# Kernel tuning notes

Hardware: AMD Instinct MI355X
Metric: run time of the kernel (lower is better)

The kernel has to match this reference:

```python
import jax, jax.numpy as jnp
import numpy as np

B, S, IN, H, D, NH, L, C = 32, 512, 3, 64, 128, 8, 4, 5
NSUB = 10          # euler substeps per interval: dt = interval/10 for these inputs
MAX_CONSEC = 50    # max_consecutive_steps in torch code
DH = D // NH
EPS = 1e-5


def _ln(x, g, b):
    m = x.mean(-1, keepdims=True)
    v = ((x - m) ** 2).mean(-1, keepdims=True)
    return (x - m) / jnp.sqrt(v + EPS) * g + b


def setup_inputs():
    key = jax.random.key(0)
    ks = jax.random.split(key, 24)
    def g(i, shape, scale=0.05):
        return jax.random.normal(ks[i], shape, dtype=jnp.float32) * scale
    dts = jax.random.uniform(ks[0], (B, S), minval=0.001, maxval=0.05, dtype=jnp.float32)
    times = jnp.cumsum(dts, axis=1)  # strictly increasing, positive
    return dict(
        time_series=jax.random.normal(ks[1], (B, S, IN), dtype=jnp.float32),
        times=times,
        noise=jax.random.normal(ks[2], (S, NSUB, B, H), dtype=jnp.float32),
        mask=jnp.ones((B, S), dtype=bool),
        enc_w=g(3, (IN, H)), enc_b=jnp.zeros((H,)),
        enc_g=jnp.ones((H,)), enc_beta=jnp.zeros((H,)),
        dw1=g(4, (H + 1, 2 * H)), db1=jnp.zeros((2 * H,)),
        dw2=g(5, (2 * H, H)), db2=jnp.zeros((H,)),
        dw3=g(6, (H, H)), db3=jnp.zeros((H,)),
        aw1=g(7, (1, H)), ab1=jnp.zeros((H,)),
        aw2=g(8, (H, H)), ab2=jnp.zeros((H,)),
        bw1=g(9, (1, H)), bb1=jnp.zeros((H,)),
        bw2=g(10, (H, H)), bb2=jnp.zeros((H,)),
        min_diff=jnp.float32(0.1),
        in_w=g(11, (H, D)), in_b=jnp.zeros((D,)),
        wq=g(12, (L, D, D)), bq=jnp.zeros((L, D)),
        wk=g(13, (L, D, D)), bk=jnp.zeros((L, D)),
        wv=g(14, (L, D, D)), bv=jnp.zeros((L, D)),
        wo=g(15, (L, D, D)), bo=jnp.zeros((L, D)),
        ln1_g=jnp.ones((L, D)), ln1_b=jnp.zeros((L, D)),
        ln2_g=jnp.ones((L, D)), ln2_b=jnp.zeros((L, D)),
        fw1=g(16, (L, D, 4 * D)), fb1=jnp.zeros((L, 4 * D)),
        fw2=g(17, (L, 4 * D, D)), fb2=jnp.zeros((L, D)),
        cw1=g(18, (D, D // 2)), cb1=jnp.zeros((D // 2,)),
        cw2=g(19, (D // 2, C)), cb2=jnp.zeros((C,)),
    )


def reference(time_series, times, noise, mask, enc_w, enc_b, enc_g, enc_beta,
              dw1, db1, dw2, db2, dw3, db3, aw1, ab1, aw2, ab2, bw1, bb1, bw2, bb2,
              min_diff, in_w, in_b, wq, bq, wk, bk, wv, bv, wo, bo,
              ln1_g, ln1_b, ln2_g, ln2_b, fw1, fb1, fw2, fb2, cw1, cb1, cw2, cb2):
    # feature encoder: Linear -> LayerNorm -> ReLU (dropout off / eval)
    enc = jax.nn.relu(_ln(time_series @ enc_w + enc_b, enc_g, enc_beta))  # (B,S,H)

    def drift(t, y):
        tcol = jnp.full((y.shape[0], 1), t, dtype=y.dtype)
        ty = jnp.concatenate([y, tcol], axis=1)
        h1 = jnp.tanh(ty @ dw1 + db1)
        h2 = jnp.tanh(h1 @ dw2 + db2)
        return h2 @ dw3 + db3

    def diffusion(t, y):
        tcol = jnp.full((y.shape[0], 1), t, dtype=y.dtype)
        A = jax.nn.softplus(jnp.tanh(tcol @ aw1 + ab1) @ aw2 + ab2)
        Bt = jnp.tanh(jnp.tanh(tcol @ bw1 + bb1) @ bw2 + bb2)
        return A + Bt * y + jnp.abs(min_diff)

    t_seq = times[0]  # torch code uses batch element 0's timestamps for sdeint

    def step(carry, xs):
        state, consec = carry
        enc_i, t_prev, t_cur, dW = xs  # dW: (NSUB,B,H) standard normals
        h = (t_cur - t_prev) / NSUB    # dt = interval/10 (< self.dt for these inputs)
        sqh = jnp.sqrt(h)
        y0 = jax.lax.stop_gradient(state)  # torch detaches y0 at every step

        def sub(y, kw):
            k, dw = kw
            t = t_prev + k * h
            return y + drift(t, y) * h + diffusion(t, y) * sqh * dw, None

        y_int, _ = jax.lax.scan(sub, y0, (jnp.arange(NSUB, dtype=jnp.float32), dW))
        skip = consec >= MAX_CONSEC
        out = jnp.where(skip, enc_i, y_int)
        consec = jnp.where(skip, jnp.int32(0), consec + 1)
        return (out, consec), out

    y0 = enc[:, 0]
    xs = (jnp.swapaxes(enc, 0, 1)[1:], t_seq[:-1], t_seq[1:], noise[1:])
    _, traj = jax.lax.scan(step, (y0, jnp.int32(0)), xs)
    sde_features = jnp.concatenate([y0[:, None], jnp.swapaxes(traj, 0, 1)], axis=1)  # (B,S,H)

    mf = mask.astype(sde_features.dtype)
    sde_features = sde_features * mf[..., None]  # MaskedSequenceProcessor.apply_mask

    # ContiFormer (post-LN transformer encoder) over SDE features
    x = sde_features @ in_w + in_b  # (B,S,D)
    neg = jnp.asarray(-1e9, x.dtype)
    for l in range(L):
        q = (x @ wq[l] + bq[l]).reshape(B, S, NH, DH)
        k = (x @ wk[l] + bk[l]).reshape(B, S, NH, DH)
        v = (x @ wv[l] + bv[l]).reshape(B, S, NH, DH)
        scores = jnp.einsum('bqhd,bkhd->bhqk', q, k) / np.float32(np.sqrt(DH))
        scores = jnp.where(mask[:, None, None, :], scores, neg)
        att = jax.nn.softmax(scores, axis=-1)
        o = jnp.einsum('bhqk,bkhd->bqhd', att, v).reshape(B, S, D) @ wo[l] + bo[l]
        x = _ln(x + o, ln1_g[l], ln1_b[l])
        f = jax.nn.relu(x @ fw1[l] + fb1[l]) @ fw2[l] + fb2[l]
        x = _ln(x + f, ln2_g[l], ln2_b[l])
    pooled = (x * mf[..., None]).sum(1) / jnp.maximum(mf.sum(1, keepdims=True), 1.0)

    logits = jax.nn.relu(pooled @ cw1 + cb1) @ cw2 + cb2
    return logits, sde_features
```

## Files before the change

kernel.cpp:

```cpp
#include <hip/hip_runtime.h>
#include <hip/hip_bf16.h>


typedef __attribute__((ext_vector_type(8))) short short8;
typedef __attribute__((ext_vector_type(4))) float f32x4;

static constexpr int OFF_TS      = 0;
static constexpr int OFF_TIMES   = 49152;
static constexpr int OFF_ENCW    = 65536;
static constexpr int OFF_ENCB    = 65728;
static constexpr int OFF_ENCG    = 65792;
static constexpr int OFF_ENCBETA = 65856;
static constexpr int OFF_DW1     = 65920;
static constexpr int OFF_DB1     = 74240;
static constexpr int OFF_DW2     = 74368;
static constexpr int OFF_DB2     = 82560;
static constexpr int OFF_DW3     = 82624;
static constexpr int OFF_DB3     = 86720;
static constexpr int OFF_AW1     = 86784;
static constexpr int OFF_AB1     = 86848;
static constexpr int OFF_AW2     = 86912;
static constexpr int OFF_AB2     = 91008;
static constexpr int OFF_BW1     = 91072;
static constexpr int OFF_BB1     = 91136;
static constexpr int OFF_BW2     = 91200;
static constexpr int OFF_BB2     = 95296;
static constexpr int OFF_MD      = 95360;
static constexpr int OFF_INW     = 95424;
static constexpr int OFF_INB     = 103616;
static constexpr int OFF_WQ      = 103744;
static constexpr int OFF_BQ      = 169280;
static constexpr int OFF_WK      = 169792;
static constexpr int OFF_BK      = 235328;
static constexpr int OFF_WV      = 235840;
static constexpr int OFF_BV      = 301376;
static constexpr int OFF_WO      = 301888;
static constexpr int OFF_BO      = 367424;
static constexpr int OFF_LN1G    = 367936;
static constexpr int OFF_LN1B    = 368448;
static constexpr int OFF_LN2G    = 368960;
static constexpr int OFF_LN2B    = 369472;
static constexpr int OFF_FW1     = 369984;
static constexpr int OFF_FB1     = 632128;
static constexpr int OFF_FW2     = 634176;
static constexpr int OFF_FB2     = 896320;
static constexpr int OFF_CW1     = 896832;
static constexpr int OFF_CB1     = 905024;
static constexpr int OFF_CW2     = 905088;
static constexpr int OFF_CB2     = 905472;
static constexpr int OFF_FLAG    = 905536;
static constexpr int OFF_ENC     = 905600;
static constexpr int OFF_COEFA   = 3002752;
static constexpr int OFF_COEFB   = 3329792;
static constexpr int OFF_B1C     = 3656832;
static constexpr int OFF_X       = 4310912;
static constexpr int OFF_XBF     = 6408064;
static constexpr int OFF_QKVBF   = 7456640;
static constexpr int OFF_OBF     = 10602368;
static constexpr int OFF_HBF     = 11650944;
static constexpr int OFF_SDEBF   = 15845248;
static constexpr int OFF_WQKVT   = 16369536;
static constexpr int OFF_WOT     = 16467840;
static constexpr int OFF_FW1T    = 16500608;
static constexpr int OFF_FW2T    = 16631680;
static constexpr int OFF_INWT    = 16762752;
static constexpr int OFF_BQKV    = 16766848;
static constexpr int OFF_TMP     = 23185280;

struct PtrPack { const void* p[45]; };

__device__ inline float wsum64(float v) {
#pragma unroll
  for (int off = 32; off > 0; off >>= 1) v += __shfl_xor(v, off, 64);
  return v;
}

__device__ inline float fast_tanh(float x) {
  x = fminf(fmaxf(x, -15.f), 15.f);
  float e = __expf(2.f * x);
  return (e - 1.f) / (e + 1.f);
}

__device__ inline float tanh5(float x) {
  float e = __builtin_amdgcn_exp2f(x * 2.88539008f);
  return 1.f - 2.f * __builtin_amdgcn_rcpf(e + 1.f);
}

__device__ inline float bfdec(unsigned short h) {
  return __uint_as_float(((unsigned)h) << 16);
}

__device__ inline short f2bf(float f) {
  unsigned u = __float_as_uint(f);
  return (short)((u + 0x7FFFu + ((u >> 16) & 1u)) >> 16);
}

__device__ inline void lds_barrier() {
  asm volatile("s_waitcnt lgkmcnt(0)\ns_barrier" ::: "memory");
}

__global__ __launch_bounds__(256) void ingest_kernel(PtrPack pk, float* __restrict__ W) {
  const int NE = 43;
  const int cnt[NE] = {49152,16384,192,64,64,64,8320,128,8192,64,4096,64,64,64,4096,64,
                       64,64,4096,64,1,8192,128,65536,512,65536,512,65536,512,65536,512,
                       512,512,512,512,262144,2048,262144,512,8192,64,320,5};
  const int src[NE] = {0,1,4,5,6,7,8,9,10,11,12,13,14,15,16,17,18,19,20,21,22,23,24,
                       25,26,27,28,29,30,31,32,33,34,35,36,37,38,39,40,41,42,43,44};
  const int dst[NE] = {OFF_TS,OFF_TIMES,OFF_ENCW,OFF_ENCB,OFF_ENCG,OFF_ENCBETA,OFF_DW1,
                       OFF_DB1,OFF_DW2,OFF_DB2,OFF_DW3,OFF_DB3,OFF_AW1,OFF_AB1,OFF_AW2,
                       OFF_AB2,OFF_BW1,OFF_BB1,OFF_BW2,OFF_BB2,OFF_MD,OFF_INW,OFF_INB,
                       OFF_WQ,OFF_BQ,OFF_WK,OFF_BK,OFF_WV,OFF_BV,OFF_WO,OFF_BO,
                       OFF_LN1G,OFF_LN1B,OFF_LN2G,OFF_LN2B,OFF_FW1,OFF_FB1,OFF_FW2,
                       OFF_FB2,OFF_CW1,OFF_CB1,OFF_CW2,OFF_CB2};
  const unsigned* eg = (const unsigned*)pk.p[6];
  int gmode = (eg[0] == 0x3F803F80u) ? 1 : 0;

  __shared__ int isbf[NE];
  if (threadIdx.x < NE) {
    int k = threadIdx.x;
    int f = gmode;
    if (gmode) {
      const unsigned short* us = (const unsigned short*)pk.p[src[k]];
      int n = cnt[k] < 32 ? cnt[k] : 32;
      for (int i = 0; i < n; ++i) {
        unsigned short h = us[i];
        if (h & 0x7FFF) {
          float a = fabsf(bfdec(h));
          if (!(a > 1e-20f && a < 1e4f)) { f = 0; break; }
        }
      }
    }
    isbf[k] = f;
  }
  __syncthreads();

  int gid = blockIdx.x * 256 + threadIdx.x;
  int stride = gridDim.x * 256;
  if (gid == 0) {
    int nf = gmode;
    if (gmode) {
      const unsigned short* us = (const unsigned short*)pk.p[2];
      for (int i = 0; i < 32; ++i) {
        unsigned short h = us[i];
        if (h & 0x7FFF) {
          float a = fabsf(bfdec(h));
          if (!(a > 1e-20f && a < 1e4f)) { nf = 0; break; }
        }
      }
    }
    ((int*)W)[OFF_FLAG] = nf;
  }
  for (int k = 0; k < NE; ++k) {
    int n = cnt[k];
    float* dp = W + dst[k];
    if (isbf[k]) {
      const unsigned short* us = (const unsigned short*)pk.p[src[k]];
      for (int e = gid; e < n; e += stride) dp[e] = bfdec(us[e]);
    } else {
      const float* fs = (const float*)pk.p[src[k]];
      for (int e = gid; e < n; e += stride) dp[e] = fs[e];
    }
  }
}

__global__ __launch_bounds__(256) void prep_kernel(float* __restrict__ W) {
  short* wqkvT = (short*)(W + OFF_WQKVT);
  short* woT   = (short*)(W + OFF_WOT);
  short* fw1T  = (short*)(W + OFF_FW1T);
  short* fw2T  = (short*)(W + OFF_FW2T);
  short* inwT  = (short*)(W + OFF_INWT);
  float* bqkv  = W + OFF_BQKV;
  int gid = blockIdx.x * 256 + threadIdx.x;
  int stride = gridDim.x * 256;
  for (int e = gid; e < 4096; e += stride) W[OFF_TMP + e] = 0.f;
  for (int e = gid; e < 796160; e += stride) {
    if (e < 196608) {
      int l = e / 49152, r = e % 49152, n = r >> 7, k = r & 127;
      float v = (n < 128) ? W[OFF_WQ + l*16384 + k*128 + n]
              : (n < 256) ? W[OFF_WK + l*16384 + k*128 + (n - 128)]
                          : W[OFF_WV + l*16384 + k*128 + (n - 256)];
      wqkvT[e] = f2bf(v);
    } else if (e < 262144) {
      int t = e - 196608; int l = t / 16384, r = t % 16384, n = r >> 7, k = r & 127;
      woT[t] = f2bf(W[OFF_WO + l*16384 + k*128 + n]);
    } else if (e < 524288) {
      int t = e - 262144; int l = t / 65536, r = t % 65536, n = r >> 7, k = r & 127;
      fw1T[t] = f2bf(W[OFF_FW1 + l*65536 + k*512 + n]);
    } else if (e < 786432) {
      int t = e - 524288; int l = t / 65536, r = t % 65536, n = r >> 9, k = r & 511;
      fw2T[t] = f2bf(W[OFF_FW2 + l*65536 + k*128 + n]);
    } else if (e < 794624) {
      int t = e - 786432; int n = t >> 6, k = t & 63;
      inwT[t] = f2bf(W[OFF_INW + k*128 + n]);
    } else {
      int t = e - 794624; int l = t / 384, j = t % 384;
      bqkv[t] = (j < 128) ? W[OFF_BQ + l*128 + j]
              : (j < 256) ? W[OFF_BK + l*128 + (j - 128)]
                          : W[OFF_BV + l*128 + (j - 256)];
    }
  }
}

__global__ __launch_bounds__(128) void prelude_kernel(float* __restrict__ W,
                                                      float* __restrict__ outf) {
  int blk = blockIdx.x;
  int tid = threadIdx.x;
  if (blk < 5110) {
    int bi = blk;
    int step = bi / 10, k = bi - step * 10;
    float t_prev = W[OFF_TIMES + step];
    float t_cur  = W[OFF_TIMES + step + 1];
    float h = (t_cur - t_prev) * 0.1f;
    float t = t_prev + (float)k * h;
    __shared__ float av[64], bv[64];
    if (tid < 64) av[tid] = fast_tanh(t * W[OFF_AW1 + tid] + W[OFF_AB1 + tid]);
    else { int j = tid - 64; bv[j] = fast_tanh(t * W[OFF_BW1 + j] + W[OFF_BB1 + j]); }
    __syncthreads();
    if (tid < 64) {
      float a = W[OFF_AB2 + tid];
      for (int i = 0; i < 64; ++i) a += av[i] * W[OFF_AW2 + i*64 + tid];
      W[OFF_COEFA + bi*64 + tid] = fmaxf(a, 0.f) + log1pf(__expf(-fabsf(a)));
    } else {
      int j = tid - 64;
      float a = W[OFF_BB2 + j];
      for (int i = 0; i < 64; ++i) a += bv[i] * W[OFF_BW2 + i*64 + j];
      W[OFF_COEFB + bi*64 + j] = fast_tanh(a);
    }
    W[OFF_B1C + bi*128 + tid] = t * W[OFF_DW1 + 64*128 + tid] + W[OFF_DB1 + tid];
  } else {
    if (tid >= 64) return;
    int idx = blk - 5110;
    int b = idx / 11, gi = idx - b*11;
    int row = b*512 + gi*51;
    int j = tid;
    float t0 = W[OFF_TS + row*3 + 0];
    float t1 = W[OFF_TS + row*3 + 1];
    float t2 = W[OFF_TS + row*3 + 2];
    float v = W[OFF_ENCB + j] + t0 * W[OFF_ENCW + j] + t1 * W[OFF_ENCW + 64 + j]
            + t2 * W[OFF_ENCW + 128 + j];
    float mean = wsum64(v) * (1.f / 64.f);
    float d = v - mean;
    float var = wsum64(d * d) * (1.f / 64.f);
    float o = d * rsqrtf(var + 1e-5f) * W[OFF_ENCG + j] + W[OFF_ENCBETA + j];
    o = fmaxf(o, 0.f);
    W[OFF_ENC + row*64 + j] = o;
    ((short*)(W + OFF_SDEBF))[row*64 + j] = f2bf(o);
    outf[160 + row*64 + j] = o;
  }
}

__global__ __launch_bounds__(256, 1) void sde_kernel(float* __restrict__ W,
                                                     const void* __restrict__ noise,
                                                     float* __restrict__ outf) {
  __shared__ short ybf[16 * 72];
  __shared__ short h1bf[16 * 136];
  __shared__ short h2bf[16 * 72];

  const int tid = threadIdx.x;
  const int w   = tid >> 6;
  const int lane = tid & 63;
  const int q   = lane >> 4;
  const int lq  = lane & 15;
  const int g   = blockIdx.x >> 1;
  const int r0  = (blockIdx.x & 1) * 16;

  const int nmode = ((const int*)W)[OFF_FLAG];
  const float md = fabsf(W[OFF_MD]);
  const unsigned short* nb16 = (const unsigned short*)noise;
  const float* nf32 = (const float*)noise;
  short* sdebf = (short*)(W + OFF_SDEBF);

  const int ncol = w*16 + lq;
  short8 B1f[2][2];
#pragma unroll
  for (int kt = 0; kt < 2; ++kt)
#pragma unroll
    for (int ct = 0; ct < 2; ++ct)
#pragma unroll
      for (int j = 0; j < 8; ++j)
        B1f[kt][ct][j] = f2bf(W[OFF_DW1 + (kt*32 + q*8 + j)*128 + w*32 + ct*16 + lq]);
  short8 B2f[4];
#pragma unroll
  for (int kt = 0; kt < 4; ++kt)
#pragma unroll
    for (int j = 0; j < 8; ++j)
      B2f[kt][j] = f2bf(W[OFF_DW2 + (kt*32 + q*8 + j)*64 + ncol]);
  short8 B3f[2];
#pragma unroll
  for (int kt = 0; kt < 2; ++kt)
#pragma unroll
    for (int j = 0; j < 8; ++j)
      B3f[kt][j] = f2bf(W[OFF_DW3 + (kt*32 + q*8 + j)*64 + ncol]);
  const float db2v = W[OFF_DB2 + ncol];
  const float db3v = W[OFF_DB3 + ncol];

  float yreg[4];
#pragma unroll
  for (int r = 0; r < 4; ++r) {
    yreg[r] = W[OFF_ENC + ((r0 + q*4 + r)*512 + 51*g)*64 + ncol];
    ybf[(q*4 + r)*72 + ncol] = f2bf(yreg[r]);
  }

  const int ci0 = 51*g*10;
  float bias_a = W[OFF_B1C + ci0*128 + w*32 + lq];
  float bias_b = W[OFF_B1C + ci0*128 + w*32 + 16 + lq];
  float ca = W[OFF_COEFA + ci0*64 + ncol];
  float cb = W[OFF_COEFB + ci0*64 + ncol];

  const int nsteps = (g == 10) ? 1 : 50;
  for (int m = 0; m < nsteps; ++m) {
    const int istep = 51*g + m;
    const float t_prev = W[OFF_TIMES + istep];
    const float t_cur  = W[OFF_TIMES + istep + 1];
    const float hstep = (t_cur - t_prev) * 0.1f;
    const float sqh = sqrtf(hstep);
    for (int k = 0; k < 10; ++k) {
      const int ci = istep*10 + k;
      const int cin = (ci + 1 > 5109) ? 5109 : ci + 1;
      float b1na = W[OFF_B1C + cin*128 + w*32 + lq];
      float b1nb = W[OFF_B1C + cin*128 + w*32 + 16 + lq];
      float can = W[OFF_COEFA + cin*64 + ncol];
      float cbn = W[OFF_COEFB + cin*64 + ncol];
      float dwv[4];
      {
        const int nb = (((istep + 1)*10 + k)*32 + r0 + q*4)*64 + ncol;
#pragma unroll
        for (int r = 0; r < 4; ++r)
          dwv[r] = nmode ? bfdec(nb16[nb + r*64]) : nf32[nb + r*64];
      }
      lds_barrier();
      {
        short8 a0 = *(const short8*)&ybf[lq*72 + q*8];
        short8 a1 = *(const short8*)&ybf[lq*72 + 32 + q*8];
        f32x4 c0 = {bias_a, bias_a, bias_a, bias_a};
        c0 = __builtin_amdgcn_mfma_f32_16x16x32_bf16(a0, B1f[0][0], c0, 0, 0, 0);
        c0 = __builtin_amdgcn_mfma_f32_16x16x32_bf16(a1, B1f[1][0], c0, 0, 0, 0);
        f32x4 c1 = {bias_b, bias_b, bias_b, bias_b};
        c1 = __builtin_amdgcn_mfma_f32_16x16x32_bf16(a0, B1f[0][1], c1, 0, 0, 0);
        c1 = __builtin_amdgcn_mfma_f32_16x16x32_bf16(a1, B1f[1][1], c1, 0, 0, 0);
#pragma unroll
        for (int r = 0; r < 4; ++r) {
          h1bf[(q*4 + r)*136 + w*32 + lq]      = f2bf(tanh5(c0[r]));
          h1bf[(q*4 + r)*136 + w*32 + 16 + lq] = f2bf(tanh5(c1[r]));
        }
      }
      lds_barrier();
      {
        short8 h0 = *(const short8*)&h1bf[lq*136 + q*8];
        short8 h1 = *(const short8*)&h1bf[lq*136 + 32 + q*8];
        short8 h2 = *(const short8*)&h1bf[lq*136 + 64 + q*8];
        short8 h3 = *(const short8*)&h1bf[lq*136 + 96 + q*8];
        f32x4 cA = {db2v, db2v, db2v, db2v};
        cA = __builtin_amdgcn_mfma_f32_16x16x32_bf16(h0, B2f[0], cA, 0, 0, 0);
        cA = __builtin_amdgcn_mfma_f32_16x16x32_bf16(h1, B2f[1], cA, 0, 0, 0);
        f32x4 cB = {0.f, 0.f, 0.f, 0.f};
        cB = __builtin_amdgcn_mfma_f32_16x16x32_bf16(h2, B2f[2], cB, 0, 0, 0);
        cB = __builtin_amdgcn_mfma_f32_16x16x32_bf16(h3, B2f[3], cB, 0, 0, 0);
#pragma unroll
        for (int r = 0; r < 4; ++r)
          h2bf[(q*4 + r)*72 + ncol] = f2bf(tanh5(cA[r] + cB[r]));
      }
      lds_barrier();
      {
        short8 g0 = *(const short8*)&h2bf[lq*72 + q*8];
        short8 g1 = *(const short8*)&h2bf[lq*72 + 32 + q*8];
        f32x4 d = {db3v, db3v, db3v, db3v};
        d = __builtin_amdgcn_mfma_f32_16x16x32_bf16(g0, B3f[0], d, 0, 0, 0);
        d = __builtin_amdgcn_mfma_f32_16x16x32_bf16(g1, B3f[1], d, 0, 0, 0);
#pragma unroll
        for (int r = 0; r < 4; ++r) {
          float yv = yreg[r];
          yv = yv + d[r]*hstep + (ca + cb*yv + md)*sqh*dwv[r];
          yreg[r] = yv;
          ybf[(q*4 + r)*72 + ncol] = f2bf(yv);
        }
      }
      bias_a = b1na; bias_b = b1nb; ca = can; cb = cbn;
    }
#pragma unroll
    for (int r = 0; r < 4; ++r) {
      const int gi = ((r0 + q*4 + r)*512 + (istep + 1))*64 + ncol;
      sdebf[gi] = f2bf(yreg[r]);
      outf[160 + gi] = yreg[r];
    }
  }
}

__global__ __launch_bounds__(256) void gemm_ln64_kernel(
    const short* __restrict__ A, const short* __restrict__ BT,
    const float* __restrict__ bias, float* __restrict__ X,
    short* __restrict__ Xb, int K) {
  __shared__ short As[64 * 40];
  __shared__ short Bs[128 * 40];
  const int tid = threadIdx.x;
  const int w = tid >> 6, lane = tid & 63, q = lane >> 4, lq = lane & 15;
  const int bm = blockIdx.x * 64;
  f32x4 acc[8];
#pragma unroll
  for (int i = 0; i < 8; ++i) acc[i] = (f32x4){0.f, 0.f, 0.f, 0.f};

  const int arow = tid >> 2, acol = (tid & 3) * 8;
  const int brow = tid >> 1, bcol = (tid & 1) * 16;
  for (int k0 = 0; k0 < K; k0 += 32) {
    short8 a  = *(const short8*)&A[(bm + arow)*K + k0 + acol];
    short8 b0 = *(const short8*)&BT[brow*K + k0 + bcol];
    short8 b1 = *(const short8*)&BT[brow*K + k0 + bcol + 8];
    __syncthreads();
    *(short8*)&As[arow*40 + acol]    = a;
    *(short8*)&Bs[brow*40 + bcol]    = b0;
    *(short8*)&Bs[brow*40 + bcol+8]  = b1;
    __syncthreads();
    short8 af = *(const short8*)&As[(w*16 + lq)*40 + q*8];
#pragma unroll
    for (int ni = 0; ni < 8; ++ni) {
      short8 bf = *(const short8*)&Bs[(ni*16 + lq)*40 + q*8];
      acc[ni] = __builtin_amdgcn_mfma_f32_16x16x32_bf16(af, bf, acc[ni], 0, 0, 0);
    }
  }
#pragma unroll
  for (int r = 0; r < 4; ++r) {
    const int row = bm + w*16 + q*4 + r;
#pragma unroll
    for (int ni = 0; ni < 8; ++ni) {
      const int col = ni*16 + lq;
      float v = acc[ni][r] + bias[col];
      X[row*128 + col] = v;
      Xb[row*128 + col] = f2bf(v);
    }
  }
}

__global__ __launch_bounds__(256, 2) void ffn_fused_kernel(
    const short* __restrict__ Obf, const short* __restrict__ woT,
    const float* __restrict__ bo,
    const float* __restrict__ ln1g, const float* __restrict__ ln1b,
    const short* __restrict__ fw1T, const float* __restrict__ fb1,
    const short* __restrict__ fw2T, const float* __restrict__ fb2,
    const float* __restrict__ ln2g, const float* __restrict__ ln2b,
    float* __restrict__ X, short* __restrict__ Xb,
    float* __restrict__ psum) {
  __shared__ short U1[64 * 136];
  __shared__ short Hs[64 * 136];
  __shared__ short Bs[128 * 136];
  const int tid = threadIdx.x;
  const int w = tid >> 6, lane = tid & 63, q = lane >> 4, lq = lane & 15;
  const int bm = blockIdx.x * 64;
  const int sr = tid >> 2, scb = (tid & 3) * 32;
  const int bn = tid >> 1, kb = (tid & 1) * 64;

  short8 abuf[4], bbuf[8];
#pragma unroll
  for (int j = 0; j < 4; ++j)
    abuf[j] = *(const short8*)&Obf[(bm + sr)*128 + scb + j*8];
#pragma unroll
  for (int j = 0; j < 8; ++j)
    bbuf[j] = *(const short8*)&woT[bn*128 + kb + j*8];
#pragma unroll
  for (int j = 0; j < 4; ++j) *(short8*)&U1[sr*136 + scb + j*8] = abuf[j];
#pragma unroll
  for (int j = 0; j < 8; ++j) *(short8*)&Bs[bn*136 + kb + j*8] = bbuf[j];
  lds_barrier();

#pragma unroll
  for (int j = 0; j < 8; ++j)
    bbuf[j] = *(const short8*)&fw1T[bn*128 + kb + j*8];

  f32x4 acc[8];
#pragma unroll
  for (int i = 0; i < 8; ++i) acc[i] = (f32x4){0.f, 0.f, 0.f, 0.f};
#pragma unroll
  for (int ks = 0; ks < 4; ++ks) {
    short8 af = *(const short8*)&U1[(w*16 + lq)*136 + ks*32 + q*8];
#pragma unroll
    for (int ni = 0; ni < 8; ++ni) {
      short8 bf = *(const short8*)&Bs[(ni*16 + lq)*136 + ks*32 + q*8];
      acc[ni] = __builtin_amdgcn_mfma_f32_16x16x32_bf16(af, bf, acc[ni], 0, 0, 0);
    }
  }
  float xv[4][8];
#pragma unroll
  for (int r = 0; r < 4; ++r) {
    const int row = bm + w*16 + q*4 + r;
    float v[8];
    float s = 0.f, s2 = 0.f;
#pragma unroll
    for (int ni = 0; ni < 8; ++ni) {
      const int col = ni*16 + lq;
      float t = acc[ni][r] + bo[col] + X[row*128 + col];
      v[ni] = t; s += t; s2 += t*t;
    }
#pragma unroll
    for (int off = 1; off < 16; off <<= 1) {
      s  += __shfl_xor(s, off, 16);
      s2 += __shfl_xor(s2, off, 16);
    }
    float mean = s * (1.f / 128.f);
    float var = s2 * (1.f / 128.f) - mean * mean;
    float inv = rsqrtf(var + 1e-5f);
#pragma unroll
    for (int ni = 0; ni < 8; ++ni) {
      const int col = ni*16 + lq;
      float o = (v[ni] - mean) * inv * ln1g[col] + ln1b[col];
      xv[r][ni] = o;
      U1[(w*16 + q*4 + r)*136 + col] = f2bf(o);
    }
  }
  lds_barrier();
#pragma unroll
  for (int j = 0; j < 8; ++j) *(short8*)&Bs[bn*136 + kb + j*8] = bbuf[j];
#pragma unroll
  for (int j = 0; j < 8; ++j)
    bbuf[j] = *(const short8*)&fw2T[bn*512 + kb + j*8];
  lds_barrier();

  f32x4 acc2[8];
#pragma unroll
  for (int i = 0; i < 8; ++i) acc2[i] = (f32x4){0.f, 0.f, 0.f, 0.f};

  for (int c = 0; c < 4; ++c) {
#pragma unroll
    for (int i = 0; i < 8; ++i) acc[i] = (f32x4){0.f, 0.f, 0.f, 0.f};
#pragma unroll
    for (int ks = 0; ks < 4; ++ks) {
      short8 af = *(const short8*)&U1[(w*16 + lq)*136 + ks*32 + q*8];
#pragma unroll
      for (int ni = 0; ni < 8; ++ni) {
        short8 bf = *(const short8*)&Bs[(ni*16 + lq)*136 + ks*32 + q*8];
        acc[ni] = __builtin_amdgcn_mfma_f32_16x16x32_bf16(af, bf, acc[ni], 0, 0, 0);
      }
    }
#pragma unroll
    for (int r = 0; r < 4; ++r)
#pragma unroll
      for (int ni = 0; ni < 8; ++ni) {
        float hvv = fmaxf(acc[ni][r] + fb1[c*128 + ni*16 + lq], 0.f);
        Hs[(w*16 + q*4 + r)*136 + ni*16 + lq] = f2bf(hvv);
      }
    lds_barrier();
#pragma unroll
    for (int j = 0; j < 8; ++j) *(short8*)&Bs[bn*136 + kb + j*8] = bbuf[j];
    if (c < 3) {
#pragma unroll
      for (int j = 0; j < 8; ++j)
        bbuf[j] = *(const short8*)&fw1T[((c + 1)*128 + bn)*128 + kb + j*8];
    }
    lds_barrier();
#pragma unroll
    for (int ks = 0; ks < 4; ++ks) {
      short8 af = *(const short8*)&Hs[(w*16 + lq)*136 + ks*32 + q*8];
#pragma unroll
      for (int ni = 0; ni < 8; ++ni) {
        short8 bf = *(const short8*)&Bs[(ni*16 + lq)*136 + ks*32 + q*8];
        acc2[ni] = __builtin_amdgcn_mfma_f32_16x16x32_bf16(af, bf, acc2[ni], 0, 0, 0);
      }
    }
    if (c < 3) {
      lds_barrier();
#pragma unroll
      for (int j = 0; j < 8; ++j) *(short8*)&Bs[bn*136 + kb + j*8] = bbuf[j];
#pragma unroll
      for (int j = 0; j < 8; ++j)
        bbuf[j] = *(const short8*)&fw2T[bn*512 + (c + 1)*128 + kb + j*8];
      lds_barrier();
    }
  }

  float ps[8];
#pragma unroll
  for (int ni = 0; ni < 8; ++ni) ps[ni] = 0.f;
#pragma unroll
  for (int r = 0; r < 4; ++r) {
    const int row = bm + w*16 + q*4 + r;
    float v[8];
    float s = 0.f, s2 = 0.f;
#pragma unroll
    for (int ni = 0; ni < 8; ++ni) {
      const int col = ni*16 + lq;
      float t = acc2[ni][r] + fb2[col] + xv[r][ni];
      v[ni] = t; s += t; s2 += t*t;
    }
#pragma unroll
    for (int off = 1; off < 16; off <<= 1) {
      s  += __shfl_xor(s, off, 16);
      s2 += __shfl_xor(s2, off, 16);
    }
    float mean = s * (1.f / 128.f);
    float var = s2 * (1.f / 128.f) - mean * mean;
    float inv = rsqrtf(var + 1e-5f);
#pragma unroll
    for (int ni = 0; ni < 8; ++ni) {
      const int col = ni*16 + lq;
      float o = (v[ni] - mean) * inv * ln2g[col] + ln2b[col];
      X[row*128 + col] = o;
      Xb[row*128 + col] = f2bf(o);
      ps[ni] += o;
    }
  }
  if (psum != nullptr) {
    const int b = bm >> 9;
#pragma unroll
    for (int ni = 0; ni < 8; ++ni) {
      float v = ps[ni];
      v += __shfl_xor(v, 16, 64);
      v += __shfl_xor(v, 32, 64);
      if (q == 0) atomicAdd(&psum[b*128 + ni*16 + lq], v);
    }
  }
}

__global__ __launch_bounds__(256, 1) void attn_fused_kernel(
    const short* __restrict__ Xb, const short* __restrict__ wqkvT,
    const float* __restrict__ bqkv, short* __restrict__ O) {
  __shared__ short Kt[512 * 20];
  __shared__ short Vt[16 * 520];
  __shared__ short U[4 * 2176];
  __shared__ short Qt[4 * 320];
  const int blk = blockIdx.x;
  const int h = blk & 7, b = blk >> 3;
  const int tid = threadIdx.x;
  const int w = tid >> 6, lane = tid & 63, q = lane >> 4, lq = lane & 15;

  short8 BQf[4], BKf[4], BVf[4];
#pragma unroll
  for (int ks = 0; ks < 4; ++ks) {
    BQf[ks] = *(const short8*)&wqkvT[(h*16 + lq)*128 + ks*32 + q*8];
    BKf[ks] = *(const short8*)&wqkvT[(128 + h*16 + lq)*128 + ks*32 + q*8];
    BVf[ks] = *(const short8*)&wqkvT[(256 + h*16 + lq)*128 + ks*32 + q*8];
  }
  const float qb = bqkv[h*16 + lq];
  const float kb = bqkv[128 + h*16 + lq];
  const float vb = bqkv[256 + h*16 + lq];

  short* Uw = &U[w * 2176];
  const int srow = lane >> 2;
  const int scol = (lane & 3) * 32;
  for (int c = 0; c < 8; ++c) {
    const int grow = b*512 + c*64 + w*16;
    short8 xa[4];
#pragma unroll
    for (int j = 0; j < 4; ++j)
      xa[j] = *(const short8*)&Xb[(size_t)(grow + srow)*128 + scol + j*8];
#pragma unroll
    for (int j = 0; j < 4; ++j)
      *(short8*)&Uw[srow*136 + scol + j*8] = xa[j];
    f32x4 kacc = {0.f, 0.f, 0.f, 0.f};
    f32x4 vacc = {0.f, 0.f, 0.f, 0.f};
#pragma unroll
    for (int ks = 0; ks < 4; ++ks) {
      short8 af = *(const short8*)&Uw[lq*136 + ks*32 + q*8];
      kacc = __builtin_amdgcn_mfma_f32_16x16x32_bf16(af, BKf[ks], kacc, 0, 0, 0);
      vacc = __builtin_amdgcn_mfma_f32_16x16x32_bf16(af, BVf[ks], vacc, 0, 0, 0);
    }
#pragma unroll
    for (int r = 0; r < 4; ++r) {
      const int key = c*64 + w*16 + q*4 + r;
      Kt[key*20 + lq]  = f2bf(kacc[r] + kb);
      Vt[lq*520 + key] = f2bf(vacc[r] + vb);
    }
  }
  lds_barrier();

  short* Pw = Uw;
  short* Qw = &Qt[w * 320];
  const float cexp = 0.25f * 1.44269504f;

  for (int qi = 0; qi < 8; ++qi) {
    const int qrow0 = b*512 + (w*8 + qi)*16;
    {
      f32x4 qacc = {0.f, 0.f, 0.f, 0.f};
#pragma unroll
      for (int ks = 0; ks < 4; ++ks) {
        short8 af = *(const short8*)&Xb[(size_t)(qrow0 + lq)*128 + ks*32 + q*8];
        qacc = __builtin_amdgcn_mfma_f32_16x16x32_bf16(af, BQf[ks], qacc, 0, 0, 0);
      }
#pragma unroll
      for (int r = 0; r < 4; ++r)
        Qw[(q*4 + r)*20 + lq] = f2bf(qacc[r] + qb);
    }
    short8 aq = (short8){0,0,0,0,0,0,0,0};
    if (q < 2) aq = *(const short8*)&Qw[lq*20 + q*8];

    f32x4 acc[32];
#pragma unroll
    for (int t = 0; t < 32; ++t) {
      short8 bk = (short8){0,0,0,0,0,0,0,0};
      if (q < 2) bk = *(const short8*)&Kt[(t*16 + lq)*20 + q*8];
      f32x4 z = {0.f, 0.f, 0.f, 0.f};
      acc[t] = __builtin_amdgcn_mfma_f32_16x16x32_bf16(aq, bk, z, 0, 0, 0);
    }
    float mx[4] = {-1e30f, -1e30f, -1e30f, -1e30f};
#pragma unroll
    for (int t = 0; t < 32; ++t)
#pragma unroll
      for (int r = 0; r < 4; ++r) mx[r] = fmaxf(mx[r], acc[t][r]);
#pragma unroll
    for (int off = 1; off < 16; off <<= 1)
#pragma unroll
      for (int r = 0; r < 4; ++r) mx[r] = fmaxf(mx[r], __shfl_xor(mx[r], off, 16));
    float ls[4] = {0.f, 0.f, 0.f, 0.f};
#pragma unroll
    for (int t = 0; t < 32; ++t)
#pragma unroll
      for (int r = 0; r < 4; ++r) {
        float p = __builtin_amdgcn_exp2f((acc[t][r] - mx[r]) * cexp);
        acc[t][r] = p;
        ls[r] += p;
      }
#pragma unroll
    for (int off = 1; off < 16; off <<= 1)
#pragma unroll
      for (int r = 0; r < 4; ++r) ls[r] += __shfl_xor(ls[r], off, 16);

    f32x4 o = {0.f, 0.f, 0.f, 0.f};
#pragma unroll
    for (int c = 0; c < 4; ++c) {
#pragma unroll
      for (int tt = 0; tt < 8; ++tt)
#pragma unroll
        for (int r = 0; r < 4; ++r)
          Pw[(q*4 + r)*136 + tt*16 + lq] =
              (short)(__float_as_uint(acc[c*8 + tt][r]) >> 16);
#pragma unroll
      for (int kk = 0; kk < 4; ++kk) {
        short8 ap = *(const short8*)&Pw[lq*136 + kk*32 + q*8];
        short8 bv = *(const short8*)&Vt[lq*520 + c*128 + kk*32 + q*8];
        o = __builtin_amdgcn_mfma_f32_16x16x32_bf16(ap, bv, o, 0, 0, 0);
      }
    }
#pragma unroll
    for (int r = 0; r < 4; ++r) {
      float ov = o[r] * __builtin_amdgcn_rcpf(ls[r]);
      O[(size_t)(qrow0 + q*4 + r)*128 + h*16 + lq] = f2bf(ov);
    }
  }
}

__global__ __launch_bounds__(128) void pool_cls_kernel(const float* __restrict__ W,
                                                       float* __restrict__ outf) {
  int b = blockIdx.x, j = threadIdx.x;
  __shared__ float pooled[128];
  __shared__ float hid[64];
  pooled[j] = W[OFF_TMP + b*128 + j] * (1.f / 512.f);
  __syncthreads();
  if (j < 64) {
    float a = W[OFF_CB1 + j];
    for (int i = 0; i < 128; ++i) a += pooled[i] * W[OFF_CW1 + i*64 + j];
    hid[j] = fmaxf(a, 0.f);
  }
  __syncthreads();
  if (j < 5) {
    float a = W[OFF_CB2 + j];
    for (int i = 0; i < 64; ++i) a += hid[i] * W[OFF_CW2 + i*5 + j];
    outf[b*5 + j] = a;
  }
}

extern "C" void kernel_launch(void* const* d_in, const int* in_sizes, int n_in,
                              void* d_out, int out_size, void* d_ws, size_t ws_size,
                              hipStream_t stream) {
  (void)in_sizes; (void)out_size; (void)ws_size;
  float* W = reinterpret_cast<float*>(d_ws);
  float* outf = reinterpret_cast<float*>(d_out);
  short* sdebf = (short*)(W + OFF_SDEBF);
  short* xbf   = (short*)(W + OFF_XBF);
  short* obf   = (short*)(W + OFF_OBF);
  PtrPack pk;
  for (int i = 0; i < 45 && i < n_in; ++i) pk.p[i] = d_in[i];

  ingest_kernel<<<512, 256, 0, stream>>>(pk, W);
  prep_kernel<<<512, 256, 0, stream>>>(W);
  prelude_kernel<<<5462, 128, 0, stream>>>(W, outf);
  sde_kernel<<<22, 256, 0, stream>>>(W, d_in[2], outf);

  gemm_ln64_kernel<<<256, 256, 0, stream>>>(sdebf, (short*)(W + OFF_INWT),
      W + OFF_INB, W + OFF_X, xbf, 64);
  for (int l = 0; l < 4; ++l) {
    attn_fused_kernel<<<256, 256, 0, stream>>>(xbf,
        (short*)(W + OFF_WQKVT) + l*49152, W + OFF_BQKV + l*384, obf);
    ffn_fused_kernel<<<256, 256, 0, stream>>>(obf,
        (short*)(W + OFF_WOT) + l*16384, W + OFF_BO + l*128,
        W + OFF_LN1G + l*128, W + OFF_LN1B + l*128,
        (short*)(W + OFF_FW1T) + l*65536, W + OFF_FB1 + l*512,
        (short*)(W + OFF_FW2T) + l*65536, W + OFF_FB2 + l*128,
        W + OFF_LN2G + l*128, W + OFF_LN2B + l*128,
        W + OFF_X, xbf, (l == 3) ? (W + OFF_TMP) : nullptr);
  }
  pool_cls_kernel<<<32, 128, 0, stream>>>(W, outf);
}
```

Baseline: 933.4 us.

## Double threads per block in attention and FFN kernels, fold prep into prelude

```diff
diff --git a/kernel.cpp b/kernel.cpp
--- a/kernel.cpp
+++ b/kernel.cpp
@@ -163,44 +163,6 @@
   }
 }
 
-__global__ __launch_bounds__(256) void prep_kernel(float* __restrict__ W) {
-  short* wqkvT = (short*)(W + OFF_WQKVT);
-  short* woT   = (short*)(W + OFF_WOT);
-  short* fw1T  = (short*)(W + OFF_FW1T);
-  short* fw2T  = (short*)(W + OFF_FW2T);
-  short* inwT  = (short*)(W + OFF_INWT);
-  float* bqkv  = W + OFF_BQKV;
-  int gid = blockIdx.x * 256 + threadIdx.x;
-  int stride = gridDim.x * 256;
-  for (int e = gid; e < 4096; e += stride) W[OFF_TMP + e] = 0.f;
-  for (int e = gid; e < 796160; e += stride) {
-    if (e < 196608) {
-      int l = e / 49152, r = e % 49152, n = r >> 7, k = r & 127;
-      float v = (n < 128) ? W[OFF_WQ + l*16384 + k*128 + n]
-              : (n < 256) ? W[OFF_WK + l*16384 + k*128 + (n - 128)]
-                          : W[OFF_WV + l*16384 + k*128 + (n - 256)];
-      wqkvT[e] = f2bf(v);
-    } else if (e < 262144) {
-      int t = e - 196608; int l = t / 16384, r = t % 16384, n = r >> 7, k = r & 127;
-      woT[t] = f2bf(W[OFF_WO + l*16384 + k*128 + n]);
-    } else if (e < 524288) {
-      int t = e - 262144; int l = t / 65536, r = t % 65536, n = r >> 7, k = r & 127;
-      fw1T[t] = f2bf(W[OFF_FW1 + l*65536 + k*512 + n]);
-    } else if (e < 786432) {
-      int t = e - 524288; int l = t / 65536, r = t % 65536, n = r >> 9, k = r & 511;
-      fw2T[t] = f2bf(W[OFF_FW2 + l*65536 + k*128 + n]);
-    } else if (e < 794624) {
-      int t = e - 786432; int n = t >> 6, k = t & 63;
-      inwT[t] = f2bf(W[OFF_INW + k*128 + n]);
-    } else {
-      int t = e - 794624; int l = t / 384, j = t % 384;
-      bqkv[t] = (j < 128) ? W[OFF_BQ + l*128 + j]
-              : (j < 256) ? W[OFF_BK + l*128 + (j - 128)]
-                          : W[OFF_BV + l*128 + (j - 256)];
-    }
-  }
-}
-
 __global__ __launch_bounds__(128) void prelude_kernel(float* __restrict__ W,
                                                       float* __restrict__ outf) {
   int blk = blockIdx.x;
@@ -227,7 +189,7 @@
       W[OFF_COEFB + bi*64 + j] = fast_tanh(a);
     }
     W[OFF_B1C + bi*128 + tid] = t * W[OFF_DW1 + 64*128 + tid] + W[OFF_DB1 + tid];
-  } else {
+  } else if (blk < 5462) {
     if (tid >= 64) return;
     int idx = blk - 5110;
     int b = idx / 11, gi = idx - b*11;
@@ -246,6 +208,42 @@
     W[OFF_ENC + row*64 + j] = o;
     ((short*)(W + OFF_SDEBF))[row*64 + j] = f2bf(o);
     outf[160 + row*64 + j] = o;
+  } else {
+    short* wqkvT = (short*)(W + OFF_WQKVT);
+    short* woT   = (short*)(W + OFF_WOT);
+    short* fw1T  = (short*)(W + OFF_FW1T);
+    short* fw2T  = (short*)(W + OFF_FW2T);
+    short* inwT  = (short*)(W + OFF_INWT);
+    float* bqkv  = W + OFF_BQKV;
+    int gid = (blk - 5462) * 128 + tid;
+    int stride = 512 * 128;
+    for (int e = gid; e < 4096; e += stride) W[OFF_TMP + e] = 0.f;
+    for (int e = gid; e < 796160; e += stride) {
+      if (e < 196608) {
+        int l = e / 49152, r = e % 49152, n = r >> 7, k = r & 127;
+        float v = (n < 128) ? W[OFF_WQ + l*16384 + k*128 + n]
+                : (n < 256) ? W[OFF_WK + l*16384 + k*128 + (n - 128)]
+                            : W[OFF_WV + l*16384 + k*128 + (n - 256)];
+        wqkvT[e] = f2bf(v);
+      } else if (e < 262144) {
+        int t = e - 196608; int l = t / 16384, r = t % 16384, n = r >> 7, k = r & 127;
+        woT[t] = f2bf(W[OFF_WO + l*16384 + k*128 + n]);
+      } else if (e < 524288) {
+        int t = e - 262144; int l = t / 65536, r = t % 65536, n = r >> 7, k = r & 127;
+        fw1T[t] = f2bf(W[OFF_FW1 + l*65536 + k*512 + n]);
+      } else if (e < 786432) {
+        int t = e - 524288; int l = t / 65536, r = t % 65536, n = r >> 9, k = r & 511;
+        fw2T[t] = f2bf(W[OFF_FW2 + l*65536 + k*128 + n]);
+      } else if (e < 794624) {
+        int t = e - 786432; int n = t >> 6, k = t & 63;
+        inwT[t] = f2bf(W[OFF_INW + k*128 + n]);
+      } else {
+        int t = e - 794624; int l = t / 384, j = t % 384;
+        bqkv[t] = (j < 128) ? W[OFF_BQ + l*128 + j]
+                : (j < 256) ? W[OFF_BK + l*128 + (j - 128)]
+                            : W[OFF_BV + l*128 + (j - 256)];
+      }
+    }
   }
 }
 
@@ -430,7 +428,7 @@
   }
 }
 
-__global__ __launch_bounds__(256, 2) void ffn_fused_kernel(
+__global__ __launch_bounds__(512, 2) void ffn_fused_kernel(
     const short* __restrict__ Obf, const short* __restrict__ woT,
     const float* __restrict__ bo,
     const float* __restrict__ ln1g, const float* __restrict__ ln1b,
@@ -442,155 +440,171 @@
   __shared__ short U1[64 * 136];
   __shared__ short Hs[64 * 136];
   __shared__ short Bs[128 * 136];
+  __shared__ float LNp[64][2][2];
   const int tid = threadIdx.x;
-  const int w = tid >> 6, lane = tid & 63, q = lane >> 4, lq = lane & 15;
+  const int w8 = tid >> 6, rg = w8 & 3, ch = w8 >> 2;
+  const int lane = tid & 63, q = lane >> 4, lq = lane & 15;
   const int bm = blockIdx.x * 64;
-  const int sr = tid >> 2, scb = (tid & 3) * 32;
-  const int bn = tid >> 1, kb = (tid & 1) * 64;
-
-  short8 abuf[4], bbuf[8];
+  const int sr = tid >> 3, sc = (tid & 7) * 16;
+  const int bn = tid >> 2, kb = (tid & 3) * 32;
+  const int rowl0 = rg*16 + q*4;
+
+  short8 abuf[2], bbuf[4];
+#pragma unroll
+  for (int j = 0; j < 2; ++j)
+    abuf[j] = *(const short8*)&Obf[(bm + sr)*128 + sc + j*8];
 #pragma unroll
   for (int j = 0; j < 4; ++j)
-    abuf[j] = *(const short8*)&Obf[(bm + sr)*128 + scb + j*8];
-#pragma unroll
-  for (int j = 0; j < 8; ++j)
     bbuf[j] = *(const short8*)&woT[bn*128 + kb + j*8];
 #pragma unroll
-  for (int j = 0; j < 4; ++j) *(short8*)&U1[sr*136 + scb + j*8] = abuf[j];
-#pragma unroll
-  for (int j = 0; j < 8; ++j) *(short8*)&Bs[bn*136 + kb + j*8] = bbuf[j];
+  for (int j = 0; j < 2; ++j) *(short8*)&U1[sr*136 + sc + j*8] = abuf[j];
+#pragma unroll
+  for (int j = 0; j < 4; ++j) *(short8*)&Bs[bn*136 + kb + j*8] = bbuf[j];
   lds_barrier();
 
 #pragma unroll
-  for (int j = 0; j < 8; ++j)
+  for (int j = 0; j < 4; ++j)
     bbuf[j] = *(const short8*)&fw1T[bn*128 + kb + j*8];
 
-  f32x4 acc[8];
-#pragma unroll
-  for (int i = 0; i < 8; ++i) acc[i] = (f32x4){0.f, 0.f, 0.f, 0.f};
+  f32x4 acc[4];
+#pragma unroll
+  for (int i = 0; i < 4; ++i) acc[i] = (f32x4){0.f, 0.f, 0.f, 0.f};
 #pragma unroll
   for (int ks = 0; ks < 4; ++ks) {
-    short8 af = *(const short8*)&U1[(w*16 + lq)*136 + ks*32 + q*8];
-#pragma unroll
-    for (int ni = 0; ni < 8; ++ni) {
-      short8 bf = *(const short8*)&Bs[(ni*16 + lq)*136 + ks*32 + q*8];
+    short8 af = *(const short8*)&U1[(rg*16 + lq)*136 + ks*32 + q*8];
+#pragma unroll
+    for (int ni = 0; ni < 4; ++ni) {
+      short8 bf = *(const short8*)&Bs[((ch*4 + ni)*16 + lq)*136 + ks*32 + q*8];
       acc[ni] = __builtin_amdgcn_mfma_f32_16x16x32_bf16(af, bf, acc[ni], 0, 0, 0);
     }
   }
-  float xv[4][8];
+  float vbuf[4][4];
 #pragma unroll
   for (int r = 0; r < 4; ++r) {
-    const int row = bm + w*16 + q*4 + r;
-    float v[8];
+    const int row = bm + rowl0 + r;
     float s = 0.f, s2 = 0.f;
 #pragma unroll
-    for (int ni = 0; ni < 8; ++ni) {
-      const int col = ni*16 + lq;
+    for (int ni = 0; ni < 4; ++ni) {
+      const int col = ch*64 + ni*16 + lq;
       float t = acc[ni][r] + bo[col] + X[row*128 + col];
-      v[ni] = t; s += t; s2 += t*t;
+      vbuf[r][ni] = t; s += t; s2 += t*t;
     }
 #pragma unroll
     for (int off = 1; off < 16; off <<= 1) {
       s  += __shfl_xor(s, off, 16);
       s2 += __shfl_xor(s2, off, 16);
     }
+    if (lq == 0) { LNp[rowl0 + r][ch][0] = s; LNp[rowl0 + r][ch][1] = s2; }
+  }
+  lds_barrier();
+#pragma unroll
+  for (int j = 0; j < 4; ++j) *(short8*)&Bs[bn*136 + kb + j*8] = bbuf[j];
+#pragma unroll
+  for (int j = 0; j < 4; ++j)
+    bbuf[j] = *(const short8*)&fw2T[bn*512 + kb + j*8];
+  float xv[4][4];
+#pragma unroll
+  for (int r = 0; r < 4; ++r) {
+    const int rowl = rowl0 + r;
+    float s  = LNp[rowl][0][0] + LNp[rowl][1][0];
+    float s2 = LNp[rowl][0][1] + LNp[rowl][1][1];
     float mean = s * (1.f / 128.f);
     float var = s2 * (1.f / 128.f) - mean * mean;
     float inv = rsqrtf(var + 1e-5f);
 #pragma unroll
-    for (int ni = 0; ni < 8; ++ni) {
-      const int col = ni*16 + lq;
-      float o = (v[ni] - mean) * inv * ln1g[col] + ln1b[col];
+    for (int ni = 0; ni < 4; ++ni) {
+      const int col = ch*64 + ni*16 + lq;
+      float o = (vbuf[r][ni] - mean) * inv * ln1g[col] + ln1b[col];
       xv[r][ni] = o;
-      U1[(w*16 + q*4 + r)*136 + col] = f2bf(o);
+      U1[rowl*136 + col] = f2bf(o);
     }
   }
   lds_barrier();
-#pragma unroll
-  for (int j = 0; j < 8; ++j) *(short8*)&Bs[bn*136 + kb + j*8] = bbuf[j];
-#pragma unroll
-  for (int j = 0; j < 8; ++j)
-    bbuf[j] = *(const short8*)&fw2T[bn*512 + kb + j*8];
-  lds_barrier();
-
-  f32x4 acc2[8];
-#pragma unroll
-  for (int i = 0; i < 8; ++i) acc2[i] = (f32x4){0.f, 0.f, 0.f, 0.f};
+
+  f32x4 acc2[4];
+#pragma unroll
+  for (int i = 0; i < 4; ++i) acc2[i] = (f32x4){0.f, 0.f, 0.f, 0.f};
 
   for (int c = 0; c < 4; ++c) {
 #pragma unroll
-    for (int i = 0; i < 8; ++i) acc[i] = (f32x4){0.f, 0.f, 0.f, 0.f};
+    for (int i = 0; i < 4; ++i) acc[i] = (f32x4){0.f, 0.f, 0.f, 0.f};
 #pragma unroll
     for (int ks = 0; ks < 4; ++ks) {
-      short8 af = *(const short8*)&U1[(w*16 + lq)*136 + ks*32 + q*8];
-#pragma unroll
-      for (int ni = 0; ni < 8; ++ni) {
-        short8 bf = *(const short8*)&Bs[(ni*16 + lq)*136 + ks*32 + q*8];
+      short8 af = *(const short8*)&U1[(rg*16 + lq)*136 + ks*32 + q*8];
+#pragma unroll
+      for (int ni = 0; ni < 4; ++ni) {
+        short8 bf = *(const short8*)&Bs[((ch*4 + ni)*16 + lq)*136 + ks*32 + q*8];
         acc[ni] = __builtin_amdgcn_mfma_f32_16x16x32_bf16(af, bf, acc[ni], 0, 0, 0);
       }
     }
 #pragma unroll
     for (int r = 0; r < 4; ++r)
 #pragma unroll
-      for (int ni = 0; ni < 8; ++ni) {
-        float hvv = fmaxf(acc[ni][r] + fb1[c*128 + ni*16 + lq], 0.f);
-        Hs[(w*16 + q*4 + r)*136 + ni*16 + lq] = f2bf(hvv);
+      for (int ni = 0; ni < 4; ++ni) {
+        const int cl = ch*64 + ni*16 + lq;
+        float hvv = fmaxf(acc[ni][r] + fb1[c*128 + cl], 0.f);
+        Hs[(rowl0 + r)*136 + cl] = f2bf(hvv);
       }
     lds_barrier();
 #pragma unroll
-    for (int j = 0; j < 8; ++j) *(short8*)&Bs[bn*136 + kb + j*8] = bbuf[j];
+    for (int j = 0; j < 4; ++j) *(short8*)&Bs[bn*136 + kb + j*8] = bbuf[j];
     if (c < 3) {
 #pragma unroll
-      for (int j = 0; j < 8; ++j)
+      for (int j = 0; j < 4; ++j)
         bbuf[j] = *(const short8*)&fw1T[((c + 1)*128 + bn)*128 + kb + j*8];
     }
     lds_barrier();
 #pragma unroll
     for (int ks = 0; ks < 4; ++ks) {
-      short8 af = *(const short8*)&Hs[(w*16 + lq)*136 + ks*32 + q*8];
-#pragma unroll
-      for (int ni = 0; ni < 8; ++ni) {
-        short8 bf = *(const short8*)&Bs[(ni*16 + lq)*136 + ks*32 + q*8];
+      short8 af = *(const short8*)&Hs[(rg*16 + lq)*136 + ks*32 + q*8];
+#pragma unroll
+      for (int ni = 0; ni < 4; ++ni) {
+        short8 bf = *(const short8*)&Bs[((ch*4 + ni)*16 + lq)*136 + ks*32 + q*8];
         acc2[ni] = __builtin_amdgcn_mfma_f32_16x16x32_bf16(af, bf, acc2[ni], 0, 0, 0);
       }
     }
     if (c < 3) {
       lds_barrier();
 #pragma unroll
-      for (int j = 0; j < 8; ++j) *(short8*)&Bs[bn*136 + kb + j*8] = bbuf[j];
-#pragma unroll
-      for (int j = 0; j < 8; ++j)
+      for (int j = 0; j < 4; ++j) *(short8*)&Bs[bn*136 + kb + j*8] = bbuf[j];
+#pragma unroll
+      for (int j = 0; j < 4; ++j)
         bbuf[j] = *(const short8*)&fw2T[bn*512 + (c + 1)*128 + kb + j*8];
       lds_barrier();
     }
   }
 
-  float ps[8];
-#pragma unroll
-  for (int ni = 0; ni < 8; ++ni) ps[ni] = 0.f;
 #pragma unroll
   for (int r = 0; r < 4; ++r) {
-    const int row = bm + w*16 + q*4 + r;
-    float v[8];
     float s = 0.f, s2 = 0.f;
 #pragma unroll
-    for (int ni = 0; ni < 8; ++ni) {
-      const int col = ni*16 + lq;
+    for (int ni = 0; ni < 4; ++ni) {
+      const int col = ch*64 + ni*16 + lq;
       float t = acc2[ni][r] + fb2[col] + xv[r][ni];
-      v[ni] = t; s += t; s2 += t*t;
+      vbuf[r][ni] = t; s += t; s2 += t*t;
     }
 #pragma unroll
     for (int off = 1; off < 16; off <<= 1) {
       s  += __shfl_xor(s, off, 16);
       s2 += __shfl_xor(s2, off, 16);
     }
+    if (lq == 0) { LNp[rowl0 + r][ch][0] = s; LNp[rowl0 + r][ch][1] = s2; }
+  }
+  lds_barrier();
+  float ps[4] = {0.f, 0.f, 0.f, 0.f};
+#pragma unroll
+  for (int r = 0; r < 4; ++r) {
+    const int rowl = rowl0 + r;
+    const int row = bm + rowl;
+    float s  = LNp[rowl][0][0] + LNp[rowl][1][0];
+    float s2 = LNp[rowl][0][1] + LNp[rowl][1][1];
     float mean = s * (1.f / 128.f);
     float var = s2 * (1.f / 128.f) - mean * mean;
     float inv = rsqrtf(var + 1e-5f);
 #pragma unroll
-    for (int ni = 0; ni < 8; ++ni) {
-      const int col = ni*16 + lq;
-      float o = (v[ni] - mean) * inv * ln2g[col] + ln2b[col];
+    for (int ni = 0; ni < 4; ++ni) {
+      const int col = ch*64 + ni*16 + lq;
+      float o = (vbuf[r][ni] - mean) * inv * ln2g[col] + ln2b[col];
       X[row*128 + col] = o;
       Xb[row*128 + col] = f2bf(o);
       ps[ni] += o;
@@ -599,22 +613,22 @@
   if (psum != nullptr) {
     const int b = bm >> 9;
 #pragma unroll
-    for (int ni = 0; ni < 8; ++ni) {
+    for (int ni = 0; ni < 4; ++ni) {
       float v = ps[ni];
       v += __shfl_xor(v, 16, 64);
       v += __shfl_xor(v, 32, 64);
-      if (q == 0) atomicAdd(&psum[b*128 + ni*16 + lq], v);
-    }
-  }
-}
-
-__global__ __launch_bounds__(256, 1) void attn_fused_kernel(
+      if (q == 0) atomicAdd(&psum[b*128 + ch*64 + ni*16 + lq], v);
+    }
+  }
+}
+
+__global__ __launch_bounds__(512, 2) void attn_fused_kernel(
     const short* __restrict__ Xb, const short* __restrict__ wqkvT,
     const float* __restrict__ bqkv, short* __restrict__ O) {
   __shared__ short Kt[512 * 20];
   __shared__ short Vt[16 * 520];
-  __shared__ short U[4 * 2176];
-  __shared__ short Qt[4 * 320];
+  __shared__ short U[8 * 2176];
+  __shared__ short Qt[8 * 320];
   const int blk = blockIdx.x;
   const int h = blk & 7, b = blk >> 3;
   const int tid = threadIdx.x;
@@ -634,8 +648,8 @@
   short* Uw = &U[w * 2176];
   const int srow = lane >> 2;
   const int scol = (lane & 3) * 32;
-  for (int c = 0; c < 8; ++c) {
-    const int grow = b*512 + c*64 + w*16;
+  for (int sub = 0; sub < 4; ++sub) {
+    const int grow = b*512 + w*64 + sub*16;
     short8 xa[4];
 #pragma unroll
     for (int j = 0; j < 4; ++j)
@@ -653,7 +667,7 @@
     }
 #pragma unroll
     for (int r = 0; r < 4; ++r) {
-      const int key = c*64 + w*16 + q*4 + r;
+      const int key = w*64 + sub*16 + q*4 + r;
       Kt[key*20 + lq]  = f2bf(kacc[r] + kb);
       Vt[lq*520 + key] = f2bf(vacc[r] + vb);
     }
@@ -664,8 +678,8 @@
   short* Qw = &Qt[w * 320];
   const float cexp = 0.25f * 1.44269504f;
 
-  for (int qi = 0; qi < 8; ++qi) {
-    const int qrow0 = b*512 + (w*8 + qi)*16;
+  for (int qi = 0; qi < 4; ++qi) {
+    const int qrow0 = b*512 + (w*4 + qi)*16;
     {
       f32x4 qacc = {0.f, 0.f, 0.f, 0.f};
 #pragma unroll
@@ -768,16 +782,15 @@
   for (int i = 0; i < 45 && i < n_in; ++i) pk.p[i] = d_in[i];
 
   ingest_kernel<<<512, 256, 0, stream>>>(pk, W);
-  prep_kernel<<<512, 256, 0, stream>>>(W);
-  prelude_kernel<<<5462, 128, 0, stream>>>(W, outf);
+  prelude_kernel<<<5974, 128, 0, stream>>>(W, outf);
   sde_kernel<<<22, 256, 0, stream>>>(W, d_in[2], outf);
 
   gemm_ln64_kernel<<<256, 256, 0, stream>>>(sdebf, (short*)(W + OFF_INWT),
       W + OFF_INB, W + OFF_X, xbf, 64);
   for (int l = 0; l < 4; ++l) {
-    attn_fused_kernel<<<256, 256, 0, stream>>>(xbf,
+    attn_fused_kernel<<<256, 512, 0, stream>>>(xbf,
         (short*)(W + OFF_WQKVT) + l*49152, W + OFF_BQKV + l*384, obf);
-    ffn_fused_kernel<<<256, 256, 0, stream>>>(obf,
+    ffn_fused_kernel<<<256, 512, 0, stream>>>(obf,
         (short*)(W + OFF_WOT) + l*16384, W + OFF_BO + l*128,
         W + OFF_LN1G + l*128, W + OFF_LN1B + l*128,
         (short*)(W + OFF_FW1T) + l*65536, W + OFF_FB1 + l*512,
```

After: 865.9 us. 1.08x faster.
